# Kernel optimization log

Measured on AMD Instinct MI355X. Metric: run time of the kernel, lower is better.

## Reference

```python
import jax, jax.numpy as jnp
import numpy as np
import math

B, L, D, H = 4, 2048, 768, 6
HD = D // H  # head_dim = 128

def setup_inputs() -> dict:
    key = jax.random.key(0)
    ks = jax.random.split(key, 9)
    s = 0.02
    return {
        "x": jax.random.normal(ks[0], (B, L, D), dtype=jnp.float32),
        "Wq": jax.random.normal(ks[1], (D, D), dtype=jnp.float32) * s,
        "bq": jnp.zeros((D,), dtype=jnp.float32),
        "Wk": jax.random.normal(ks[2], (D, D), dtype=jnp.float32) * s,
        "bk": jnp.zeros((D,), dtype=jnp.float32),
        "Wv": jax.random.normal(ks[3], (D, D), dtype=jnp.float32) * s,
        "bv": jnp.zeros((D,), dtype=jnp.float32),
        "Wo": jax.random.normal(ks[4], (D, D), dtype=jnp.float32) * s,
        "bo": jnp.zeros((D,), dtype=jnp.float32),
    }

def _split_heads(t):
    # [b, l, h*d] -> [b, h, l, d]
    b, l, _ = t.shape
    return t.reshape(b, l, H, HD).transpose(0, 2, 1, 3)

def reference(x, Wq, bq, Wk, bk, Wv, bv, Wo, bo):
    q = _split_heads(x @ Wq + bq)
    k = _split_heads(x @ Wk + bk)
    v = _split_heads(x @ Wv + bv)
    scores = jnp.einsum("bhqd,bhkd->bhqk", q, k) / math.sqrt(HD)
    # Original builds jnp.tril(ones, k=1) and fills mask==0 positions; it
    # mistakenly used +inf there, which yields NaN — we use -inf (intended
    # masking math) while keeping the same tril(k=1) pattern.
    l = x.shape[1]
    mask = jnp.tril(jnp.ones((l, l), dtype=bool), k=1)
    logits = jnp.where(mask, scores, -jnp.inf)
    attn = jax.nn.softmax(logits, axis=-1)
    out = jnp.einsum("bhqk,bhkd->bhqd", attn, v)
    out = out.transpose(0, 2, 1, 3).reshape(x.shape[0], l, D)
    # dropout in eval/deterministic mode: identity
    return out @ Wo + bo
```

## Files before the change

kernel.cpp:

```cpp
#include <hip/hip_runtime.h>
#include <math.h>

#define HEADS 6
#define SEQ   2048
#define DIM   768
#define HDIM  128
#define BATCH 4
#define MTOT  (BATCH*SEQ)
#define NKV   (SEQ/32)

typedef float  f32x4   __attribute__((ext_vector_type(4)));
typedef float  f32x16  __attribute__((ext_vector_type(16)));
typedef __bf16 bf16x8  __attribute__((ext_vector_type(8)));
typedef __bf16 bf16x4  __attribute__((ext_vector_type(4)));
typedef float  f32x4v  __attribute__((ext_vector_type(4)));

typedef __attribute__((address_space(3))) void lds_v;
typedef __attribute__((address_space(1))) void gbl_v;

__device__ __forceinline__ f32x4 mfma16(bf16x8 a, bf16x8 b, f32x4 c) {
    return __builtin_amdgcn_mfma_f32_16x16x32_bf16(a, b, c, 0, 0, 0);
}
__device__ __forceinline__ f32x16 mfma32(bf16x8 a, bf16x8 b, f32x16 c) {
    return __builtin_amdgcn_mfma_f32_32x32x16_bf16(a, b, c, 0, 0, 0);
}
__device__ __forceinline__ unsigned int cvtpk(float lo, float hi) {
    unsigned int r;
    asm("v_cvt_pk_bf16_f32 %0, %1, %2" : "=v"(r) : "v"(lo), "v"(hi));
    return r;
}

__global__ __launch_bounds__(256) void cast_x_kernel(const float* __restrict__ x,
                                                     __bf16* __restrict__ xb) {
    int i = (blockIdx.x * 256 + threadIdx.x) * 4;
    f32x4v v = *(const f32x4v*)(x + i);
    bf16x4 o;
    o[0] = (__bf16)v[0]; o[1] = (__bf16)v[1];
    o[2] = (__bf16)v[2]; o[3] = (__bf16)v[3];
    *(bf16x4*)(xb + i) = o;
}

__global__ __launch_bounds__(256) void transpose_w_kernel(
    const float* __restrict__ W0, const float* __restrict__ W1,
    const float* __restrict__ W2, const float* __restrict__ W3,
    __bf16* __restrict__ T0, __bf16* __restrict__ T1,
    __bf16* __restrict__ T2, __bf16* __restrict__ T3) {
    __shared__ float tile[32][33];
    const float* W; __bf16* T;
    if      (blockIdx.z == 0) { W = W0; T = T0; }
    else if (blockIdx.z == 1) { W = W1; T = T1; }
    else if (blockIdx.z == 2) { W = W2; T = T2; }
    else                      { W = W3; T = T3; }
    int n0 = blockIdx.x * 32, k0 = blockIdx.y * 32;
    int tx = threadIdx.x & 31, ty = threadIdx.x >> 5;
#pragma unroll
    for (int i = 0; i < 4; ++i)
        tile[ty + i*8][tx] = W[(size_t)(k0 + ty + i*8) * DIM + n0 + tx];
    __syncthreads();
#pragma unroll
    for (int i = 0; i < 4; ++i)
        T[(size_t)(n0 + ty + i*8) * DIM + k0 + tx] = (__bf16)tile[tx][ty + i*8];
}

#define GEMM_PIPE(A_PTR, B_PTR, NKSTEP)                                           \
    __shared__ __align__(16) __bf16 As[3][128 * 32];                              \
    __shared__ __align__(16) __bf16 Bs[3][128 * 32];                              \
    const int tid  = threadIdx.x;                                                 \
    const int wave = tid >> 6, lane = tid & 63;                                   \
    const int l16  = lane & 15, lh = lane >> 4;                                   \
    const int wr = wave >> 1, wc = wave & 1;                                      \
    f32x4 acc[4][4] = {};                                                         \
    auto stage = [&](int buf, int step) {                                         \
        const int k0 = step * 32;                                                 \
        _Pragma("unroll")                                                         \
        for (int ci = 0; ci < 4; ++ci) {                                          \
            int c = wave * 4 + ci;                                                \
            int t = c & 7;                                                        \
            int e = (t * 64 + lane) * 8;                                          \
            int r = e >> 5, kk = e & 31;                                          \
            const __bf16* gp = (c < 8) ? ((A_PTR) + (size_t)(m0 + r) * DIM + k0 + kk) \
                                       : ((B_PTR) + (size_t)(n0 + r) * DIM + k0 + kk); \
            __bf16* lp = (c < 8 ? As[buf] : Bs[buf]) + t * 512;                   \
            __builtin_amdgcn_global_load_lds((const gbl_v*)gp, (lds_v*)lp, 16, 0, 0); \
        }                                                                         \
    };                                                                            \
    stage(0, 0); stage(1, 1);                                                     \
    asm volatile("s_waitcnt vmcnt(4)" ::: "memory");                              \
    __builtin_amdgcn_s_barrier();                                                 \
    for (int t = 0; t < (NKSTEP); ++t) {                                          \
        const int cur = t % 3;                                                    \
        if (t + 2 < (NKSTEP)) stage((t + 2) % 3, t + 2);                          \
        bf16x8 af[4], bfr[4];                                                     \
        _Pragma("unroll")                                                         \
        for (int i = 0; i < 4; ++i)                                               \
            af[i] = *(const bf16x8*)&As[cur][(wr*64 + i*16 + l16) * 32 + lh*8];   \
        _Pragma("unroll")                                                         \
        for (int j = 0; j < 4; ++j)                                               \
            bfr[j] = *(const bf16x8*)&Bs[cur][(wc*64 + j*16 + l16) * 32 + lh*8];  \
        __builtin_amdgcn_s_setprio(1);                                            \
        _Pragma("unroll")                                                         \
        for (int i = 0; i < 4; ++i)                                               \
            _Pragma("unroll")                                                     \
            for (int j = 0; j < 4; ++j)                                           \
                acc[i][j] = mfma16(af[i], bfr[j], acc[i][j]);                     \
        __builtin_amdgcn_s_setprio(0);                                            \
        if (t + 2 < (NKSTEP))      asm volatile("s_waitcnt vmcnt(4)" ::: "memory"); \
        else if (t + 1 < (NKSTEP)) asm volatile("s_waitcnt vmcnt(0)" ::: "memory"); \
        __builtin_amdgcn_s_barrier();                                             \
    }

__global__ __launch_bounds__(256) void gemm_qkv(const __bf16* __restrict__ A,
                                                const __bf16* __restrict__ Wcat,
                                                const float* __restrict__ bq,
                                                const float* __restrict__ bk,
                                                const float* __restrict__ bv,
                                                __bf16* __restrict__ Qb,
                                                __bf16* __restrict__ Kb,
                                                __bf16* __restrict__ Vt) {
    const int bn = blockIdx.x % (2304 / 128), bm = blockIdx.x / (2304 / 128);
    const int m0 = bm * 128, n0 = bn * 128;
    GEMM_PIPE(A, Wcat, 24)

    const int sel = n0 / DIM;
    const float* bias = sel == 0 ? bq : (sel == 1 ? bk : bv);
#pragma unroll
    for (int i = 0; i < 4; ++i) {
        int row = m0 + wr*64 + i*16 + lh*4;
#pragma unroll
        for (int j = 0; j < 4; ++j) {
            int col  = n0 + wc*64 + j*16 + l16;
            int lcol = col - sel * DIM;
            float bvv = bias[lcol];
            if (sel < 2) {
                __bf16* o = (sel == 0) ? Qb : Kb;
#pragma unroll
                for (int r = 0; r < 4; ++r)
                    o[(size_t)(row + r) * DIM + lcol] = (__bf16)(acc[i][j][r] + bvv);
            } else {
                int bb = row >> 11, ll = row & (SEQ - 1);
                int hh = lcol >> 7, dd = lcol & (HDIM - 1);
                bf16x4 pk;
#pragma unroll
                for (int r = 0; r < 4; ++r) pk[r] = (__bf16)(acc[i][j][r] + bvv);
                *(bf16x4*)&Vt[((size_t)((bb*HEADS + hh) * HDIM + dd)) * SEQ + ll] = pk;
            }
        }
    }
}

__global__ __launch_bounds__(256) void gemm_out(const __bf16* __restrict__ A,
                                                const __bf16* __restrict__ Bt,
                                                const float* __restrict__ bias,
                                                float* __restrict__ outp) {
    const int bn = blockIdx.x % (DIM / 128), bm = blockIdx.x / (DIM / 128);
    const int m0 = bm * 128, n0 = bn * 128;
    GEMM_PIPE(A, Bt, 24)

#pragma unroll
    for (int i = 0; i < 4; ++i) {
        int row = m0 + wr*64 + i*16 + lh*4;
#pragma unroll
        for (int j = 0; j < 4; ++j) {
            int col = n0 + wc*64 + j*16 + l16;
            float bv = bias[col];
#pragma unroll
            for (int r = 0; r < 4; ++r)
                outp[(size_t)(row + r) * DIM + col] = acc[i][j][r] + bv;
        }
    }
}

__global__ __launch_bounds__(256, 2) void attn_kernel(
    const __bf16* __restrict__ Q, const __bf16* __restrict__ K,
    const __bf16* __restrict__ Vt,
    __bf16* __restrict__ po, float* __restrict__ pm, float* __restrict__ pl,
    __bf16* __restrict__ Ob, int ks) {
    __shared__ __align__(16) __bf16 Ks[2][32 * 128];
    const int lane = threadIdx.x & 63, wv = threadIdx.x >> 6;
    const int l32 = lane & 31, hi = lane >> 5;
    const int id  = blockIdx.x;
    const int xcd = id & 7;
    const int idx = id >> 3;
    const int bh_l = idx % 3, rem = idx / 3;
    const int c = rem % ks, tl = rem / ks;
    const int tile = (tl & 1) ? (15 - (tl >> 1)) : (tl >> 1);
    const int bh = xcd + 8 * bh_l;
    const int b = bh / HEADS, h = bh - b * HEADS;
    const int qw0 = tile * 128 + wv * 32;
    const float qs = 0.12751674770951932f;

    bf16x8 qfr[8];
    {
        const __bf16* qp = Q + (size_t)(b*SEQ + qw0 + l32) * DIM + h*HDIM + hi*8;
#pragma unroll
        for (int cc = 0; cc < 8; ++cc) {
            bf16x8 v = *(const bf16x8*)(qp + cc*16);
            bf16x8 sv;
#pragma unroll
            for (int e = 0; e < 8; ++e) sv[e] = (__bf16)((float)v[e] * qs);
            qfr[cc] = sv;
        }
    }

    const __bf16* kgb = K  + (size_t)(b*SEQ) * DIM + h*HDIM;
    const __bf16* vgb = Vt + (size_t)bh * HDIM * SEQ;

    auto stage = [&](int buf, int kb) {
        const int kbase = kb * 32;
#pragma unroll
        for (int s = 0; s < 2; ++s) {
            const int j = wv * 2 + s;
            const int row = j * 4 + (lane >> 4);
            const int c16 = (lane & 15) ^ (row & 7);
            const __bf16* gp = kgb + (size_t)(kbase + row) * DIM + c16 * 8;
            __builtin_amdgcn_global_load_lds((const gbl_v*)gp,
                (lds_v*)&Ks[buf][j * 512], 16, 0, 0);
        }
    };

    f32x16 o[4] = {};
    float mx = -INFINITY, lsum = 0.f;
    const int nkb = min(4 * tile + 5, NKV);
    const int cnt = (nkb - c + ks - 1) / ks;

    stage(0, c);
    int cur = 0;
    for (int i = 0; i < cnt; ++i) {
        const int kb = c + i * ks;
        const int kbase = kb * 32;
        if (i + 1 < cnt) {
            stage(cur ^ 1, kb + ks);
            asm volatile("s_waitcnt vmcnt(2)" ::: "memory");
        } else {
            asm volatile("s_waitcnt vmcnt(0)" ::: "memory");
        }
        __builtin_amdgcn_s_barrier();

        if (kbase <= qw0 + 32) {
            f32x16 s = {};
            __builtin_amdgcn_s_setprio(1);
#pragma unroll
            for (int cc = 0; cc < 8; ++cc) {
                const int c8 = ((cc << 1) | hi) ^ (l32 & 7);
                bf16x8 kf = *(const bf16x8*)&Ks[cur][l32 * 128 + c8 * 8];
                s = mfma32(kf, qfr[cc], s);
            }
            __builtin_amdgcn_s_setprio(0);
            bf16x8 vf[8];
#pragma unroll
            for (int db = 0; db < 4; ++db)
#pragma unroll
                for (int kc = 0; kc < 2; ++kc)
                    vf[db*2 + kc] = *(const bf16x8*)(vgb +
                        (size_t)(db*32 + l32) * SEQ + kbase + kc*16 + hi*8);

            float p[16];
#pragma unroll
            for (int r = 0; r < 16; ++r) p[r] = s[r];
            if (kbase + 30 > qw0) {
                const int q1 = qw0 + l32 + 1;
#pragma unroll
                for (int r = 0; r < 16; ++r) {
                    const int key = kbase + (r & 3) + 8*(r >> 2) + 4*hi;
                    if (key > q1) p[r] = -INFINITY;
                }
            }
            float m0 = p[0];
#pragma unroll
            for (int r = 1; r < 16; ++r) m0 = fmaxf(m0, p[r]);
            m0 = fmaxf(m0, __shfl_xor(m0, 32));
            const bool defer = __all(m0 <= mx + 8.f && mx > -3e38f);
            if (!defer) {
                const float mnew = fmaxf(mx, m0);
                const float resc = (mx < mnew) ? exp2f(mx - mnew) : 1.0f;
                lsum *= resc;
#pragma unroll
                for (int db = 0; db < 4; ++db)
#pragma unroll
                    for (int r = 0; r < 16; ++r) o[db][r] *= resc;
                mx = mnew;
            }
            const float mref = (mx == -INFINITY) ? 0.f : mx;
#pragma unroll
            for (int r = 0; r < 16; ++r) p[r] = exp2f(p[r] - mref);
            float rs = 0.f;
#pragma unroll
            for (int r = 0; r < 16; ++r) rs += p[r];
            rs += __shfl_xor(rs, 32);
            lsum += rs;
            union { unsigned int u[4]; bf16x8 v; } pw[2];
#pragma unroll
            for (int kc = 0; kc < 2; ++kc) {
                unsigned int X = cvtpk(p[8*kc + 0], p[8*kc + 1]);
                unsigned int Y = cvtpk(p[8*kc + 4], p[8*kc + 5]);
                asm("v_permlane32_swap_b32 %0, %1" : "+v"(X), "+v"(Y));
                unsigned int X2 = cvtpk(p[8*kc + 2], p[8*kc + 3]);
                unsigned int Y2 = cvtpk(p[8*kc + 6], p[8*kc + 7]);
                asm("v_permlane32_swap_b32 %0, %1" : "+v"(X2), "+v"(Y2));
                pw[kc].u[0] = X; pw[kc].u[1] = X2; pw[kc].u[2] = Y; pw[kc].u[3] = Y2;
            }
            __builtin_amdgcn_s_setprio(1);
#pragma unroll
            for (int db = 0; db < 4; ++db) {
                o[db] = mfma32(vf[db*2 + 0], pw[0].v, o[db]);
                o[db] = mfma32(vf[db*2 + 1], pw[1].v, o[db]);
            }
            __builtin_amdgcn_s_setprio(0);
        }
        __builtin_amdgcn_s_barrier();
        cur ^= 1;
    }

    if (ks == 1) {
        const float inv = 1.0f / lsum;
        __bf16* op = Ob + (size_t)(b*SEQ + qw0 + l32) * DIM + h*HDIM + hi*4;
#pragma unroll
        for (int db = 0; db < 4; ++db)
#pragma unroll
            for (int g = 0; g < 4; ++g) {
                bf16x4 pk;
#pragma unroll
                for (int r = 0; r < 4; ++r) pk[r] = (__bf16)(o[db][g*4 + r] * inv);
                *(bf16x4*)(op + db*32 + g*8) = pk;
            }
    } else {
        const int pid = (bh * 16 + tile) * ks + c;
        const int lq  = wv * 32 + l32;
        __bf16* pop = po + ((size_t)pid * 128 + lq) * HDIM + hi*4;
#pragma unroll
        for (int db = 0; db < 4; ++db)
#pragma unroll
            for (int g = 0; g < 4; ++g) {
                bf16x4 pk;
#pragma unroll
                for (int r = 0; r < 4; ++r) pk[r] = (__bf16)o[db][g*4 + r];
                *(bf16x4*)(pop + db*32 + g*8) = pk;
            }
        if (hi == 0) {
            pm[(size_t)pid * 128 + lq] = mx;
            pl[(size_t)pid * 128 + lq] = lsum;
        }
    }
}

__global__ __launch_bounds__(256) void merge_kernel(const __bf16* __restrict__ po,
    const float* __restrict__ pm, const float* __restrict__ pl,
    __bf16* __restrict__ Ob, int ks) {
    const int id = blockIdx.x;
    const int bh = id >> 4, tile = id & 15;
    const int b = bh / HEADS, h = bh - b * HEADS;
    const int lq = threadIdx.x >> 1;
    const int d0 = (threadIdx.x & 1) * 64;
    const int pb = id * ks;
    float M = -INFINITY;
    for (int cc = 0; cc < ks; ++cc) M = fmaxf(M, pm[(size_t)(pb + cc) * 128 + lq]);
    float L = 0.f, w[2] = {0.f, 0.f};
    for (int cc = 0; cc < ks; ++cc) {
        w[cc] = exp2f(pm[(size_t)(pb + cc) * 128 + lq] - M);
        L += w[cc] * pl[(size_t)(pb + cc) * 128 + lq];
    }
    const float invL = 1.0f / L;
    __bf16* op = Ob + (size_t)(b*SEQ + tile*128 + lq) * DIM + h*HDIM;
#pragma unroll
    for (int d = 0; d < 64; d += 8) {
        float acc[8] = {};
        for (int cc = 0; cc < ks; ++cc) {
            bf16x8 v = *(const bf16x8*)&po[((size_t)(pb + cc) * 128 + lq) * HDIM + d0 + d];
            const float wc = w[cc];
#pragma unroll
            for (int e = 0; e < 8; ++e) acc[e] += wc * (float)v[e];
        }
        bf16x8 ov;
#pragma unroll
        for (int e = 0; e < 8; ++e) ov[e] = (__bf16)(acc[e] * invL);
        *(bf16x8*)(op + d0 + d) = ov;
    }
}

extern "C" void kernel_launch(void* const* d_in, const int* in_sizes, int n_in,
                              void* d_out, int out_size, void* d_ws, size_t ws_size,
                              hipStream_t stream) {
    const float* x  = (const float*)d_in[0];
    const float* Wq = (const float*)d_in[1];
    const float* bq = (const float*)d_in[2];
    const float* Wk = (const float*)d_in[3];
    const float* bk = (const float*)d_in[4];
    const float* Wv = (const float*)d_in[5];
    const float* bv = (const float*)d_in[6];
    const float* Wo = (const float*)d_in[7];
    const float* bo = (const float*)d_in[8];

    char* p = (char*)d_ws;
    const size_t SZ_X = (size_t)MTOT * DIM * 2;
    const size_t SZ_W = (size_t)DIM * DIM * 2;
    __bf16* xb   = (__bf16*)p; p += SZ_X;
    __bf16* Wcat = (__bf16*)p; p += 3 * SZ_W;
    __bf16* Wto  = (__bf16*)p; p += SZ_W;
    __bf16* Qb   = (__bf16*)p; p += SZ_X;
    __bf16* Kb   = (__bf16*)p; p += SZ_X;
    __bf16* Vt   = (__bf16*)p; p += SZ_X;
    __bf16* Ob   = (__bf16*)p; p += SZ_X;

    const size_t base = (size_t)(p - (char*)d_ws);
    const size_t SZ_PO = (size_t)24 * 16 * 2 * 128 * HDIM * 2;
    const size_t SZ_PM = (size_t)24 * 16 * 2 * 128 * 4;
    const int ks = (ws_size >= base + SZ_PO + 2 * SZ_PM) ? 2 : 1;
    __bf16* po = (__bf16*)p;            p += SZ_PO;
    float*  pmv = (float*)p;            p += SZ_PM;
    float*  plv = (float*)p;

    cast_x_kernel<<<(MTOT * DIM) / 1024, 256, 0, stream>>>(x, xb);
    transpose_w_kernel<<<dim3(DIM/32, DIM/32, 4), 256, 0, stream>>>(
        Wq, Wk, Wv, Wo,
        Wcat, Wcat + (size_t)DIM*DIM, Wcat + (size_t)2*DIM*DIM, Wto);

    gemm_qkv<<<(MTOT/128) * (2304/128), 256, 0, stream>>>(xb, Wcat, bq, bk, bv, Qb, Kb, Vt);

    attn_kernel<<<8 * 3 * 16 * ks, 256, 0, stream>>>(Qb, Kb, Vt, po, pmv, plv, Ob, ks);
    if (ks == 2)
        merge_kernel<<<24 * 16, 256, 0, stream>>>(po, pmv, plv, Ob, ks);

    gemm_out<<<(MTOT/128) * (DIM/128), 256, 0, stream>>>(Ob, Wto, bo, (float*)d_out);
}
```

Measured before the change: 192.8 us.

## Split attention into single-wave blocks per 32-query tile, dropping LDS K staging

The attention kernel now launches one 64-thread wave per 32-query tile instead of four waves sharing a 128-query tile. Each wave loads K fragments straight from global memory rather than staging them through double-buffered LDS with barriers. The causal key range and the merge kernel's indexing are resized to the finer tiles. This removes barrier synchronisation and the shared-tile causal over-fetch, and gives finer load balance. The cost is that K reuse across waves and the async load pipeline are lost, so global and L2 traffic for K goes up.

```diff
diff --git a/kernel.cpp b/kernel.cpp
--- a/kernel.cpp
+++ b/kernel.cpp
@@ -170,23 +170,22 @@
     }
 }
 
-__global__ __launch_bounds__(256, 2) void attn_kernel(
+__global__ __launch_bounds__(64, 3) void attn_kernel(
     const __bf16* __restrict__ Q, const __bf16* __restrict__ K,
     const __bf16* __restrict__ Vt,
     __bf16* __restrict__ po, float* __restrict__ pm, float* __restrict__ pl,
     __bf16* __restrict__ Ob, int ks) {
-    __shared__ __align__(16) __bf16 Ks[2][32 * 128];
-    const int lane = threadIdx.x & 63, wv = threadIdx.x >> 6;
+    const int lane = threadIdx.x;
     const int l32 = lane & 31, hi = lane >> 5;
     const int id  = blockIdx.x;
     const int xcd = id & 7;
     const int idx = id >> 3;
     const int bh_l = idx % 3, rem = idx / 3;
     const int c = rem % ks, tl = rem / ks;
-    const int tile = (tl & 1) ? (15 - (tl >> 1)) : (tl >> 1);
+    const int tile = (tl & 1) ? (63 - (tl >> 1)) : (tl >> 1);
     const int bh = xcd + 8 * bh_l;
     const int b = bh / HEADS, h = bh - b * HEADS;
-    const int qw0 = tile * 128 + wv * 32;
+    const int qw0 = tile * 32;
     const float qs = 0.12751674770951932f;
 
     bf16x8 qfr[8];
@@ -205,110 +204,83 @@
     const __bf16* kgb = K  + (size_t)(b*SEQ) * DIM + h*HDIM;
     const __bf16* vgb = Vt + (size_t)bh * HDIM * SEQ;
 
-    auto stage = [&](int buf, int kb) {
-        const int kbase = kb * 32;
-#pragma unroll
-        for (int s = 0; s < 2; ++s) {
-            const int j = wv * 2 + s;
-            const int row = j * 4 + (lane >> 4);
-            const int c16 = (lane & 15) ^ (row & 7);
-            const __bf16* gp = kgb + (size_t)(kbase + row) * DIM + c16 * 8;
-            __builtin_amdgcn_global_load_lds((const gbl_v*)gp,
-                (lds_v*)&Ks[buf][j * 512], 16, 0, 0);
-        }
-    };
-
     f32x16 o[4] = {};
     float mx = -INFINITY, lsum = 0.f;
-    const int nkb = min(4 * tile + 5, NKV);
+    const int nkb = min(tile + 2, NKV);
     const int cnt = (nkb - c + ks - 1) / ks;
 
-    stage(0, c);
-    int cur = 0;
     for (int i = 0; i < cnt; ++i) {
         const int kb = c + i * ks;
         const int kbase = kb * 32;
-        if (i + 1 < cnt) {
-            stage(cur ^ 1, kb + ks);
-            asm volatile("s_waitcnt vmcnt(2)" ::: "memory");
-        } else {
-            asm volatile("s_waitcnt vmcnt(0)" ::: "memory");
-        }
-        __builtin_amdgcn_s_barrier();
-
-        if (kbase <= qw0 + 32) {
-            f32x16 s = {};
-            __builtin_amdgcn_s_setprio(1);
-#pragma unroll
-            for (int cc = 0; cc < 8; ++cc) {
-                const int c8 = ((cc << 1) | hi) ^ (l32 & 7);
-                bf16x8 kf = *(const bf16x8*)&Ks[cur][l32 * 128 + c8 * 8];
-                s = mfma32(kf, qfr[cc], s);
+        bf16x8 kf[8];
+        const __bf16* kp = kgb + (size_t)(kbase + l32) * DIM + hi*8;
+#pragma unroll
+        for (int cc = 0; cc < 8; ++cc) kf[cc] = *(const bf16x8*)(kp + cc*16);
+        f32x16 s = {};
+        __builtin_amdgcn_s_setprio(1);
+#pragma unroll
+        for (int cc = 0; cc < 8; ++cc) s = mfma32(kf[cc], qfr[cc], s);
+        __builtin_amdgcn_s_setprio(0);
+        bf16x8 vf[8];
+#pragma unroll
+        for (int db = 0; db < 4; ++db)
+#pragma unroll
+            for (int kc = 0; kc < 2; ++kc)
+                vf[db*2 + kc] = *(const bf16x8*)(vgb +
+                    (size_t)(db*32 + l32) * SEQ + kbase + kc*16 + hi*8);
+
+        float p[16];
+#pragma unroll
+        for (int r = 0; r < 16; ++r) p[r] = s[r];
+        if (kbase + 30 > qw0) {
+            const int q1 = qw0 + l32 + 1;
+#pragma unroll
+            for (int r = 0; r < 16; ++r) {
+                const int key = kbase + (r & 3) + 8*(r >> 2) + 4*hi;
+                if (key > q1) p[r] = -INFINITY;
             }
-            __builtin_amdgcn_s_setprio(0);
-            bf16x8 vf[8];
+        }
+        float m0 = p[0];
+#pragma unroll
+        for (int r = 1; r < 16; ++r) m0 = fmaxf(m0, p[r]);
+        m0 = fmaxf(m0, __shfl_xor(m0, 32));
+        const bool defer = __all(m0 <= mx + 8.f && mx > -3e38f);
+        if (!defer) {
+            const float mnew = fmaxf(mx, m0);
+            const float resc = (mx < mnew) ? exp2f(mx - mnew) : 1.0f;
+            lsum *= resc;
 #pragma unroll
             for (int db = 0; db < 4; ++db)
 #pragma unroll
-                for (int kc = 0; kc < 2; ++kc)
-                    vf[db*2 + kc] = *(const bf16x8*)(vgb +
-                        (size_t)(db*32 + l32) * SEQ + kbase + kc*16 + hi*8);
-
-            float p[16];
-#pragma unroll
-            for (int r = 0; r < 16; ++r) p[r] = s[r];
-            if (kbase + 30 > qw0) {
-                const int q1 = qw0 + l32 + 1;
-#pragma unroll
-                for (int r = 0; r < 16; ++r) {
-                    const int key = kbase + (r & 3) + 8*(r >> 2) + 4*hi;
-                    if (key > q1) p[r] = -INFINITY;
-                }
-            }
-            float m0 = p[0];
-#pragma unroll
-            for (int r = 1; r < 16; ++r) m0 = fmaxf(m0, p[r]);
-            m0 = fmaxf(m0, __shfl_xor(m0, 32));
-            const bool defer = __all(m0 <= mx + 8.f && mx > -3e38f);
-            if (!defer) {
-                const float mnew = fmaxf(mx, m0);
-                const float resc = (mx < mnew) ? exp2f(mx - mnew) : 1.0f;
-                lsum *= resc;
-#pragma unroll
-                for (int db = 0; db < 4; ++db)
-#pragma unroll
-                    for (int r = 0; r < 16; ++r) o[db][r] *= resc;
-                mx = mnew;
-            }
-            const float mref = (mx == -INFINITY) ? 0.f : mx;
-#pragma unroll
-            for (int r = 0; r < 16; ++r) p[r] = exp2f(p[r] - mref);
-            float rs = 0.f;
-#pragma unroll
-            for (int r = 0; r < 16; ++r) rs += p[r];
-            rs += __shfl_xor(rs, 32);
-            lsum += rs;
-            union { unsigned int u[4]; bf16x8 v; } pw[2];
-#pragma unroll
-            for (int kc = 0; kc < 2; ++kc) {
-                unsigned int X = cvtpk(p[8*kc + 0], p[8*kc + 1]);
-                unsigned int Y = cvtpk(p[8*kc + 4], p[8*kc + 5]);
-                asm("v_permlane32_swap_b32 %0, %1" : "+v"(X), "+v"(Y));
-                unsigned int X2 = cvtpk(p[8*kc + 2], p[8*kc + 3]);
-                unsigned int Y2 = cvtpk(p[8*kc + 6], p[8*kc + 7]);
-                asm("v_permlane32_swap_b32 %0, %1" : "+v"(X2), "+v"(Y2));
-                pw[kc].u[0] = X; pw[kc].u[1] = X2; pw[kc].u[2] = Y; pw[kc].u[3] = Y2;
-            }
-            __builtin_amdgcn_s_setprio(1);
-#pragma unroll
-            for (int db = 0; db < 4; ++db) {
-                o[db] = mfma32(vf[db*2 + 0], pw[0].v, o[db]);
-                o[db] = mfma32(vf[db*2 + 1], pw[1].v, o[db]);
-            }
-            __builtin_amdgcn_s_setprio(0);
-        }
-        __builtin_amdgcn_s_barrier();
-        cur ^= 1;
+                for (int r = 0; r < 16; ++r) o[db][r] *= resc;
+            mx = mnew;
+        }
+        const float mref = (mx == -INFINITY) ? 0.f : mx;
+#pragma unroll
+        for (int r = 0; r < 16; ++r) p[r] = exp2f(p[r] - mref);
+        float rs = 0.f;
+#pragma unroll
+        for (int r = 0; r < 16; ++r) rs += p[r];
+        rs += __shfl_xor(rs, 32);
+        lsum += rs;
+        union { unsigned int u[4]; bf16x8 v; } pw[2];
+#pragma unroll
+        for (int kc = 0; kc < 2; ++kc) {
+            unsigned int X = cvtpk(p[8*kc + 0], p[8*kc + 1]);
+            unsigned int Y = cvtpk(p[8*kc + 4], p[8*kc + 5]);
+            asm("v_permlane32_swap_b32 %0, %1" : "+v"(X), "+v"(Y));
+            unsigned int X2 = cvtpk(p[8*kc + 2], p[8*kc + 3]);
+            unsigned int Y2 = cvtpk(p[8*kc + 6], p[8*kc + 7]);
+            asm("v_permlane32_swap_b32 %0, %1" : "+v"(X2), "+v"(Y2));
+            pw[kc].u[0] = X; pw[kc].u[1] = X2; pw[kc].u[2] = Y; pw[kc].u[3] = Y2;
+        }
+        __builtin_amdgcn_s_setprio(1);
+#pragma unroll
+        for (int db = 0; db < 4; ++db) {
+            o[db] = mfma32(vf[db*2 + 0], pw[0].v, o[db]);
+            o[db] = mfma32(vf[db*2 + 1], pw[1].v, o[db]);
+        }
+        __builtin_amdgcn_s_setprio(0);
     }
 
     if (ks == 1) {
@@ -324,9 +296,8 @@
                 *(bf16x4*)(op + db*32 + g*8) = pk;
             }
     } else {
-        const int pid = (bh * 16 + tile) * ks + c;
-        const int lq  = wv * 32 + l32;
-        __bf16* pop = po + ((size_t)pid * 128 + lq) * HDIM + hi*4;
+        const int pid = (bh * 64 + tile) * ks + c;
+        __bf16* pop = po + ((size_t)pid * 32 + l32) * HDIM + hi*4;
 #pragma unroll
         for (int db = 0; db < 4; ++db)
 #pragma unroll
@@ -337,35 +308,35 @@
                 *(bf16x4*)(pop + db*32 + g*8) = pk;
             }
         if (hi == 0) {
-            pm[(size_t)pid * 128 + lq] = mx;
-            pl[(size_t)pid * 128 + lq] = lsum;
-        }
-    }
-}
-
-__global__ __launch_bounds__(256) void merge_kernel(const __bf16* __restrict__ po,
+            pm[(size_t)pid * 32 + l32] = mx;
+            pl[(size_t)pid * 32 + l32] = lsum;
+        }
+    }
+}
+
+__global__ __launch_bounds__(128) void merge_kernel(const __bf16* __restrict__ po,
     const float* __restrict__ pm, const float* __restrict__ pl,
     __bf16* __restrict__ Ob, int ks) {
     const int id = blockIdx.x;
-    const int bh = id >> 4, tile = id & 15;
+    const int bh = id >> 6, tile = id & 63;
     const int b = bh / HEADS, h = bh - b * HEADS;
-    const int lq = threadIdx.x >> 1;
-    const int d0 = (threadIdx.x & 1) * 64;
+    const int lq = threadIdx.x >> 2;
+    const int d0 = (threadIdx.x & 3) * 32;
     const int pb = id * ks;
     float M = -INFINITY;
-    for (int cc = 0; cc < ks; ++cc) M = fmaxf(M, pm[(size_t)(pb + cc) * 128 + lq]);
+    for (int cc = 0; cc < ks; ++cc) M = fmaxf(M, pm[(size_t)(pb + cc) * 32 + lq]);
     float L = 0.f, w[2] = {0.f, 0.f};
     for (int cc = 0; cc < ks; ++cc) {
-        w[cc] = exp2f(pm[(size_t)(pb + cc) * 128 + lq] - M);
-        L += w[cc] * pl[(size_t)(pb + cc) * 128 + lq];
+        w[cc] = exp2f(pm[(size_t)(pb + cc) * 32 + lq] - M);
+        L += w[cc] * pl[(size_t)(pb + cc) * 32 + lq];
     }
     const float invL = 1.0f / L;
-    __bf16* op = Ob + (size_t)(b*SEQ + tile*128 + lq) * DIM + h*HDIM;
-#pragma unroll
-    for (int d = 0; d < 64; d += 8) {
+    __bf16* op = Ob + (size_t)(b*SEQ + tile*32 + lq) * DIM + h*HDIM;
+#pragma unroll
+    for (int d = 0; d < 32; d += 8) {
         float acc[8] = {};
         for (int cc = 0; cc < ks; ++cc) {
-            bf16x8 v = *(const bf16x8*)&po[((size_t)(pb + cc) * 128 + lq) * HDIM + d0 + d];
+            bf16x8 v = *(const bf16x8*)&po[((size_t)(pb + cc) * 32 + lq) * HDIM + d0 + d];
             const float wc = w[cc];
 #pragma unroll
             for (int e = 0; e < 8; ++e) acc[e] += wc * (float)v[e];
@@ -402,8 +373,8 @@
     __bf16* Ob   = (__bf16*)p; p += SZ_X;
 
     const size_t base = (size_t)(p - (char*)d_ws);
-    const size_t SZ_PO = (size_t)24 * 16 * 2 * 128 * HDIM * 2;
-    const size_t SZ_PM = (size_t)24 * 16 * 2 * 128 * 4;
+    const size_t SZ_PO = (size_t)24 * 64 * 2 * 32 * HDIM * 2;
+    const size_t SZ_PM = (size_t)24 * 64 * 2 * 32 * 4;
     const int ks = (ws_size >= base + SZ_PO + 2 * SZ_PM) ? 2 : 1;
     __bf16* po = (__bf16*)p;            p += SZ_PO;
     float*  pmv = (float*)p;            p += SZ_PM;
@@ -416,9 +387,9 @@
 
     gemm_qkv<<<(MTOT/128) * (2304/128), 256, 0, stream>>>(xb, Wcat, bq, bk, bv, Qb, Kb, Vt);
 
-    attn_kernel<<<8 * 3 * 16 * ks, 256, 0, stream>>>(Qb, Kb, Vt, po, pmv, plv, Ob, ks);
+    attn_kernel<<<8 * 3 * 64 * ks, 64, 0, stream>>>(Qb, Kb, Vt, po, pmv, plv, Ob, ks);
     if (ks == 2)
-        merge_kernel<<<24 * 16, 256, 0, stream>>>(po, pmv, plv, Ob, ks);
+        merge_kernel<<<24 * 64, 128, 0, stream>>>(po, pmv, plv, Ob, ks);
 
     gemm_out<<<(MTOT/128) * (DIM/128), 256, 0, stream>>>(Ob, Wto, bo, (float*)d_out);
 }
```

After: 218.2 us. 1.13x slower.
